# Performance work log

Hardware: AMD Instinct MI355X
Metric: run time of the kernel (lower is better)

The kernel has to match this reference:

```python
import jax, jax.numpy as jnp
import numpy as np

NUM_LEVELS = 16
BASE_RES = 16
MAX_RES = 2048
F_PER_LEVEL = 2
MAX_TABLE = 524288  # 2**19
N_POINTS = 1048576
# geometric resolution schedule, identical to the torch module
RESOLUTIONS = [int(BASE_RES * (MAX_RES / BASE_RES) ** (l / (NUM_LEVELS - 1))) for l in range(NUM_LEVELS)]
TABLE_SIZES = [min(r ** 3, MAX_TABLE) for r in RESOLUTIONS]


def setup_inputs() -> dict:
    key = jax.random.key(0)
    k0, k1, k2, k3 = jax.random.split(key, 4)
    coords = jax.random.uniform(k0, (N_POINTS, 3), minval=-1.0, maxval=1.0, dtype=jnp.float32)
    # hash tables init U(-1e-4, 1e-4); all padded to MAX_TABLE rows (levels with
    # smaller dense tables simply never index past TABLE_SIZES[l])
    tables = jax.random.uniform(k1, (NUM_LEVELS, MAX_TABLE, F_PER_LEVEL), minval=-1e-4, maxval=1e-4, dtype=jnp.float32)
    d_in = NUM_LEVELS * F_PER_LEVEL  # 32
    W1 = jax.random.normal(k2, (d_in, 128), dtype=jnp.float32) * (2.0 / (d_in + 128)) ** 0.5
    b1 = jnp.zeros((128,), dtype=jnp.float32)
    W2 = jax.random.normal(k3, (128, 64), dtype=jnp.float32) * (2.0 / (128 + 64)) ** 0.5
    b2 = jnp.zeros((64,), dtype=jnp.float32)
    return {"coords": coords, "tables": tables, "W1": W1, "b1": b1, "W2": W2, "b2": b2}


def _hash_gather(coords, tables):
    # coords: [N, 3] in [-1, 1] -> normalized to [0, 1]
    c = (coords + 1.0) * 0.5
    feats = []
    for l in range(NUM_LEVELS):
        R = RESOLUTIONS[l]
        T = TABLE_SIZES[l]
        d = jnp.clip(jnp.floor(c * R).astype(jnp.int32), 0, R - 1).astype(jnp.uint32)  # [N, 3]
        # (x*R^2 + y*R + z) % T in uint32. Wraparound mod 2^32 only occurs at the
        # finest levels where T = 2^19 divides 2^32, so the result stays exact.
        idx = (d[:, 0] * jnp.uint32(R * R) + d[:, 1] * jnp.uint32(R) + d[:, 2]) % jnp.uint32(T)
        feats.append(tables[l][idx.astype(jnp.int32)])  # [N, F_PER_LEVEL]
    return jnp.concatenate(feats, axis=-1)  # [N, 32], level-major


def reference(coords, tables, W1, b1, W2, b2):
    x = _hash_gather(coords, tables)              # [N, 32]
    h = jax.nn.relu(x @ W1 + b1)                  # [N, 128]
    return h @ W2 + b2                            # [N, 64]
```

## Files before the change

### kernel.cpp

```cpp
#include <hip/hip_runtime.h>
#include <stdint.h>


typedef __attribute__((ext_vector_type(8))) __bf16 bf16x8;
typedef __attribute__((ext_vector_type(4))) float  f32x4;
typedef __attribute__((ext_vector_type(2))) float  f32x2;

#define NPTS   1048576
#define NTILES 65536

__device__ __forceinline__ unsigned pack_bf16(float x, float y) {
  __bf16 a = (__bf16)x, b = (__bf16)y;
  unsigned short ua, ub;
  __builtin_memcpy(&ua, &a, 2);
  __builtin_memcpy(&ub, &b, 2);
  return (unsigned)ua | ((unsigned)ub << 16);
}

__global__ __launch_bounds__(256) void tconv_prep_kernel(
    const float* __restrict__ coords, const float* __restrict__ tables,
    const float* __restrict__ W1, const float* __restrict__ W2,
    unsigned* __restrict__ tb2, unsigned* __restrict__ xw,
    short* __restrict__ w1p, short* __restrict__ w2p)
{
  constexpr unsigned Rt[5] = {16u,22u,30u,42u,58u};
  if (blockIdx.x < 1024) {
    int p0 = blockIdx.x * 1024 + threadIdx.x;
#pragma unroll
    for (int i = 0; i < 4; ++i) {
      int p = p0 + (i << 8);
      float u0 = (coords[3*p+0] + 1.0f) * 0.5f;
      float u1 = (coords[3*p+1] + 1.0f) * 0.5f;
      float u2 = (coords[3*p+2] + 1.0f) * 0.5f;
#pragma unroll
      for (int lv = 0; lv < 5; ++lv) {
        const unsigned R = Rt[lv];
        const unsigned Rm1 = R - 1u;
        unsigned d0 = (unsigned)(int)(u0 * (float)R); if (d0 > Rm1) d0 = Rm1;
        unsigned d1 = (unsigned)(int)(u1 * (float)R); if (d1 > Rm1) d1 = Rm1;
        unsigned d2 = (unsigned)(int)(u2 * (float)R); if (d2 > Rm1) d2 = Rm1;
        unsigned idx = d0*(R*R) + d1*R + d2;
        f32x2 f = *(const f32x2*)(tables + ((size_t)lv << 20) + (size_t)idx*2u);
        xw[((size_t)lv << 20) + p] = pack_bf16(f.x, f.y);
      }
    }
    return;
  }
  if (blockIdx.x < 6656) {
    int e0 = 5*524288 + ((int)(blockIdx.x - 1024) * 256 + (int)threadIdx.x) * 4;
#pragma unroll
    for (int i = 0; i < 4; ++i) {
      int e = e0 + i;
      f32x2 f = *(const f32x2*)(tables + (size_t)e * 2);
      tb2[e] = pack_bf16(f.x, f.y);
    }
    return;
  }
  int tid = (blockIdx.x - 6656) * 256 + threadIdx.x;
  int l = tid & 63;
  int g = l >> 4;
  int c = l & 15;
  if (tid < 512) {
    int t = tid >> 6;
    bf16x8 v;
#pragma unroll
    for (int j = 0; j < 8; ++j)
      v[j] = (__bf16)W1[(8*g + j)*128 + 16*t + c];
    *(bf16x8*)(w1p + (size_t)(t*64 + l)*8) = v;
  } else if (tid < 1536) {
    int e = (tid - 512) >> 6;
    int mt = e >> 2, ks = e & 3;
    bf16x8 v;
#pragma unroll
    for (int j = 0; j < 8; ++j)
      v[j] = (__bf16)W2[(32*ks + 16*(j>>2) + 4*g + (j&3))*64 + 16*mt + c];
    *(bf16x8*)(w2p + (size_t)(e*64 + l)*8) = v;
  }
}

__global__ __launch_bounds__(256) void gather_kernel(
    const float* __restrict__ coords, const unsigned* __restrict__ tb2,
    unsigned* __restrict__ xw)
{
  constexpr unsigned Rt[16] = {16u,22u,30u,42u,58u,80u,111u,153u,
                               212u,294u,406u,561u,776u,1072u,1482u,2048u};
  const int xcd = blockIdx.x & 7;
  const int j   = blockIdx.x >> 3;
  int ghi = xcd * 1408 + j;
  int lv = 5 + (ghi >> 10);
  int chunk = ghi & 1023;

  const unsigned R = Rt[lv];
  const float fR = (float)R;
  const unsigned RR = R * R;
  const unsigned Rm1 = R - 1u;
  const unsigned M = (lv >= 6) ? 0x7FFFFu : 0xFFFFFFFFu;
  const unsigned* tb = tb2 + ((size_t)lv << 19);
  unsigned* xp = xw + ((size_t)lv << 20);

  int p0 = chunk * 1024 + threadIdx.x;
#pragma unroll
  for (int i = 0; i < 4; ++i) {
    int p = p0 + (i << 8);
    float u0 = (coords[3*p+0] + 1.0f) * 0.5f;
    float u1 = (coords[3*p+1] + 1.0f) * 0.5f;
    float u2 = (coords[3*p+2] + 1.0f) * 0.5f;
    unsigned d0 = (unsigned)(int)(u0 * fR); if (d0 > Rm1) d0 = Rm1;
    unsigned d1 = (unsigned)(int)(u1 * fR); if (d1 > Rm1) d1 = Rm1;
    unsigned d2 = (unsigned)(int)(u2 * fR); if (d2 > Rm1) d2 = Rm1;
    unsigned idx = (d0*RR + d1*R + d2) & M;
    xp[p] = tb[idx];
  }
}

__global__ __launch_bounds__(256, 4) void mlp_kernel(
    const unsigned* __restrict__ xw,
    const float* __restrict__ b1, const float* __restrict__ b2,
    const short* __restrict__ w1p, const short* __restrict__ w2p,
    float* __restrict__ out)
{
  const int l = threadIdx.x & 63;
  const int g = l >> 4;
  const int c = l & 15;
  const int w = threadIdx.x >> 6;

  __shared__ float obuf[4][16][68];

  bf16x8 w1f[8];
#pragma unroll
  for (int t = 0; t < 8; ++t)
    w1f[t] = *(const bf16x8*)(w1p + (size_t)(t*64 + l)*8);

  const int base = blockIdx.x * 4 + w;

  unsigned gx[2][4];
#pragma unroll
  for (int it = 0; it < 2; ++it) {
    int p = (base + it*32768)*16 + c;
#pragma unroll
    for (int q = 0; q < 4; ++q)
      gx[it][q] = xw[((size_t)(4*g + q) << 20) + p];
  }

#pragma unroll
  for (int it = 0; it < 2; ++it) {
    union { bf16x8 v; unsigned u[4]; } X;
#pragma unroll
    for (int q = 0; q < 4; ++q) X.u[q] = gx[it][q];
    bf16x8 xf = X.v;

    f32x4 h[8];
#pragma unroll
    for (int t = 0; t < 8; ++t) {
      h[t] = *(const f32x4*)(b1 + 16*t + 4*g);
      h[t] = __builtin_amdgcn_mfma_f32_16x16x32_bf16(w1f[t], xf, h[t], 0, 0, 0);
    }

    f32x4 o[4];
#pragma unroll
    for (int mt = 0; mt < 4; ++mt)
      o[mt] = *(const f32x4*)(b2 + 16*mt + 4*g);
#pragma unroll
    for (int ks = 0; ks < 4; ++ks) {
      bf16x8 bp;
#pragma unroll
      for (int j = 0; j < 8; ++j) {
        float v = h[2*ks + (j>>2)][j & 3];
        v = fmaxf(v, 0.0f);
        bp[j] = (__bf16)v;
      }
#pragma unroll
      for (int mt = 0; mt < 4; ++mt) {
        bf16x8 w2f = *(const bf16x8*)(w2p + (size_t)((mt*4 + ks)*64 + l)*8);
        o[mt] = __builtin_amdgcn_mfma_f32_16x16x32_bf16(w2f, bp, o[mt], 0, 0, 0);
      }
    }

    float (*ob)[68] = obuf[w];
#pragma unroll
    for (int mt = 0; mt < 4; ++mt)
      *(f32x4*)&ob[c][16*mt + 4*g] = o[mt];
    asm volatile("s_waitcnt lgkmcnt(0)" ::: "memory");
    f32x4 v[4];
#pragma unroll
    for (int s = 0; s < 4; ++s)
      v[s] = *(const f32x4*)&ob[4*s + g][4*c];
    asm volatile("" ::: "memory");
    float* op = out + (size_t)(base + it*32768) * 1024;
#pragma unroll
    for (int s = 0; s < 4; ++s)
      *(f32x4*)(op + (4*s + g)*64 + 4*c) = v[s];

    if (it < 1) asm volatile("s_waitcnt lgkmcnt(0)" ::: "memory");
  }
}

__global__ void prep_kernel(const float* __restrict__ W1, const float* __restrict__ W2,
                            short* __restrict__ w1p, short* __restrict__ w2p) {
  int tid = blockIdx.x * blockDim.x + threadIdx.x;
  int l = tid & 63;
  int g = l >> 4;
  int c = l & 15;
  if (tid < 512) {
    int t = tid >> 6;
    bf16x8 v;
#pragma unroll
    for (int j = 0; j < 8; ++j)
      v[j] = (__bf16)W1[(8*g + j)*128 + 16*t + c];
    *(bf16x8*)(w1p + (size_t)(t*64 + l)*8) = v;
  } else if (tid < 1536) {
    int e = (tid - 512) >> 6;
    int mt = e >> 2, ks = e & 3;
    bf16x8 v;
#pragma unroll
    for (int j = 0; j < 8; ++j)
      v[j] = (__bf16)W2[(32*ks + 16*(j>>2) + 4*g + (j&3))*64 + 16*mt + c];
    *(bf16x8*)(w2p + (size_t)(e*64 + l)*8) = v;
  }
}

__device__ const unsigned kRES[16] = {16u,22u,30u,42u,58u,80u,111u,153u,
                                      212u,294u,406u,561u,776u,1072u,1482u,2048u};

__global__ __launch_bounds__(256, 3) void hashgrid_mlp_kernel(
    const float* __restrict__ coords, const float* __restrict__ tables,
    const float* __restrict__ b1, const float* __restrict__ b2,
    const short* __restrict__ w1p, const short* __restrict__ w2p,
    float* __restrict__ out, int stride)
{
  const int l = threadIdx.x & 63;
  const int g = l >> 4;
  const int c = l & 15;

  unsigned Rq[4], RRq[4], Mq[4]; float fRq[4];
#pragma unroll
  for (int q = 0; q < 4; ++q) {
    int lv = 4*g + q;
    unsigned R = kRES[lv];
    Rq[q] = R; RRq[q] = R*R; fRq[q] = (float)R;
    Mq[q] = (lv >= 6) ? 0x7FFFFu : 0xFFFFFFFFu;
  }
  const float* tb = tables + ((size_t)g << 22);

  bf16x8 w1f[8];
#pragma unroll
  for (int t = 0; t < 8; ++t)
    w1f[t] = *(const bf16x8*)(w1p + (size_t)(t*64 + l)*8);

  f32x2 gx[4];
  auto prefetch = [&](int tile) {
    int p = tile*16 + c;
    float u0 = (coords[3*p+0] + 1.0f) * 0.5f;
    float u1 = (coords[3*p+1] + 1.0f) * 0.5f;
    float u2 = (coords[3*p+2] + 1.0f) * 0.5f;
#pragma unroll
    for (int q = 0; q < 4; ++q) {
      unsigned Rm1 = Rq[q] - 1u;
      unsigned d0 = (unsigned)(int)(u0 * fRq[q]); if (d0 > Rm1) d0 = Rm1;
      unsigned d1 = (unsigned)(int)(u1 * fRq[q]); if (d1 > Rm1) d1 = Rm1;
      unsigned d2 = (unsigned)(int)(u2 * fRq[q]); if (d2 > Rm1) d2 = Rm1;
      unsigned idx = (d0*RRq[q] + d1*Rq[q] + d2) & Mq[q];
      gx[q] = *(const f32x2*)(tb + ((size_t)q << 20) + (size_t)idx*2u);
    }
  };

  int tile = blockIdx.x * 4 + (threadIdx.x >> 6);
  prefetch(tile);
  while (true) {
    bf16x8 xf;
#pragma unroll
    for (int q = 0; q < 4; ++q) {
      xf[2*q]   = (__bf16)gx[q].x;
      xf[2*q+1] = (__bf16)gx[q].y;
    }
    int cur = tile;
    tile += stride;
    if (tile < NTILES) prefetch(tile);

    f32x4 h[8];
#pragma unroll
    for (int t = 0; t < 8; ++t) {
      h[t] = *(const f32x4*)(b1 + 16*t + 4*g);
      h[t] = __builtin_amdgcn_mfma_f32_16x16x32_bf16(w1f[t], xf, h[t], 0, 0, 0);
    }

    f32x4 o[4];
#pragma unroll
    for (int mt = 0; mt < 4; ++mt)
      o[mt] = *(const f32x4*)(b2 + 16*mt + 4*g);
#pragma unroll
    for (int ks = 0; ks < 4; ++ks) {
      bf16x8 bp;
#pragma unroll
      for (int j = 0; j < 8; ++j) {
        float v = h[2*ks + (j>>2)][j & 3];
        v = fmaxf(v, 0.0f);
        bp[j] = (__bf16)v;
      }
#pragma unroll
      for (int mt = 0; mt < 4; ++mt) {
        bf16x8 w2f = *(const bf16x8*)(w2p + (size_t)((mt*4 + ks)*64 + l)*8);
        o[mt] = __builtin_amdgcn_mfma_f32_16x16x32_bf16(w2f, bp, o[mt], 0, 0, 0);
      }
    }

    float* op = out + (size_t)(cur*16 + c)*64 + 4*g;
#pragma unroll
    for (int mt = 0; mt < 4; ++mt)
      *(f32x4*)(op + 16*mt) = o[mt];

    if (tile >= NTILES) break;
  }
}

extern "C" void kernel_launch(void* const* d_in, const int* in_sizes, int n_in,
                              void* d_out, int out_size, void* d_ws, size_t ws_size,
                              hipStream_t stream) {
  const float* coords = (const float*)d_in[0];
  const float* tables = (const float*)d_in[1];
  const float* W1     = (const float*)d_in[2];
  const float* b1     = (const float*)d_in[3];
  const float* W2     = (const float*)d_in[4];
  const float* b2     = (const float*)d_in[5];
  float* out = (float*)d_out;

  short* w1p = (short*)d_ws;
  short* w2p = w1p + 4096;

  const size_t XW_OFF  = 32*1024;
  const size_t XW_SZ   = (size_t)NPTS * 16 * 4;
  const size_t TB2_SZ  = (size_t)16 * 524288 * 4;
  const size_t need = XW_OFF + XW_SZ + TB2_SZ;

  if (ws_size >= need) {
    unsigned* xw  = (unsigned*)((char*)d_ws + XW_OFF);
    unsigned* tb2 = (unsigned*)((char*)d_ws + XW_OFF + XW_SZ);
    tconv_prep_kernel<<<6662, 256, 0, stream>>>(coords, tables, W1, W2,
                                                tb2, xw, w1p, w2p);
    gather_kernel<<<11264, 256, 0, stream>>>(coords, tb2, xw);
    mlp_kernel<<<8192, 256, 0, stream>>>(xw, b1, b2, w1p, w2p, out);
  } else {
    prep_kernel<<<6, 256, 0, stream>>>(W1, W2, w1p, w2p);
    const int blocks = 2048;
    hashgrid_mlp_kernel<<<blocks, 256, 0, stream>>>(coords, tables, b1, b2,
                                                    w1p, w2p, out, blocks*4);
  }
}
```

Baseline: 187.1 us.

## Fuse prep, gather and MLP into one cooperative kernel with slice pipelining

Replaces the three-kernel sequence with a single cooperative persistent kernel. It runs the table conversion and prep, then splits the points into four slices, so some blocks gather level features for slice s while the others run the MLP on slice s-1, with grid-wide syncs between phases. The aim is to overlap gather-bound memory traffic with MFMA work and to remove launch gaps between kernels. The cost is several grid syncs, a fixed split between gather and MLP blocks, and host-side attribute and occupancy queries on every launch. The fused single-pass fallback for small workspaces is removed, so that case now computes nothing.

```diff
diff --git a/kernel.cpp b/kernel.cpp
--- a/kernel.cpp
+++ b/kernel.cpp
@@ -1,13 +1,22 @@
 #include <hip/hip_runtime.h>
+#include <hip/hip_cooperative_groups.h>
 #include <stdint.h>
+
+namespace cg = cooperative_groups;
 
 
 typedef __attribute__((ext_vector_type(8))) __bf16 bf16x8;
 typedef __attribute__((ext_vector_type(4))) float  f32x4;
 typedef __attribute__((ext_vector_type(2))) float  f32x2;
 
-#define NPTS   1048576
-#define NTILES 65536
+#define NPTS        1048576
+#define NTILES      65536
+#define SLICE_PTS   262144
+#define SLICE_TILES 16384
+#define XCD_CHUNKS  352
+
+__device__ const unsigned kRES[16] = {16u,22u,30u,42u,58u,80u,111u,153u,
+                                      212u,294u,406u,561u,776u,1072u,1482u,2048u};
 
 __device__ __forceinline__ unsigned pack_bf16(float x, float y) {
   __bf16 a = (__bf16)x, b = (__bf16)y;
@@ -17,13 +26,204 @@
   return (unsigned)ua | ((unsigned)ub << 16);
 }
 
+__global__ __launch_bounds__(256) void mega_kernel(
+    const float* __restrict__ coords, const float* __restrict__ tables,
+    const float* __restrict__ W1, const float* __restrict__ b1,
+    const float* __restrict__ W2, const float* __restrict__ b2,
+    unsigned* __restrict__ tb2, unsigned* __restrict__ xw,
+    short* __restrict__ w1p, short* __restrict__ w2p,
+    float* __restrict__ out, int nper, int ng)
+{
+  cg::grid_group grid = cg::this_grid();
+  const int tid = threadIdx.x;
+  const int l = tid & 63;
+  const int g = l >> 4;
+  const int c = l & 15;
+  const int w = tid >> 6;
+  const int b = blockIdx.x;
+  const int x = b & 7;
+  const int r = b >> 3;
+  const int B = gridDim.x;
+
+  __shared__ float obuf[4][16][68];
+
+  for (int u = b; u < 6662; u += B) {
+    if (u < 1024) {
+      int p0 = u * 1024 + tid;
+#pragma unroll
+      for (int i = 0; i < 4; ++i) {
+        int p = p0 + (i << 8);
+        float u0 = (coords[3*p+0] + 1.0f) * 0.5f;
+        float u1 = (coords[3*p+1] + 1.0f) * 0.5f;
+        float u2 = (coords[3*p+2] + 1.0f) * 0.5f;
+#pragma unroll
+        for (int lv = 0; lv < 5; ++lv) {
+          const unsigned R = kRES[lv];
+          const unsigned Rm1 = R - 1u;
+          unsigned d0 = (unsigned)(int)(u0 * (float)R); if (d0 > Rm1) d0 = Rm1;
+          unsigned d1 = (unsigned)(int)(u1 * (float)R); if (d1 > Rm1) d1 = Rm1;
+          unsigned d2 = (unsigned)(int)(u2 * (float)R); if (d2 > Rm1) d2 = Rm1;
+          unsigned idx = d0*(R*R) + d1*R + d2;
+          f32x2 f = *(const f32x2*)(tables + ((size_t)lv << 20) + (size_t)idx*2u);
+          xw[((size_t)lv << 20) + p] = pack_bf16(f.x, f.y);
+        }
+      }
+    } else if (u < 6656) {
+      int e0 = 5*524288 + (u - 1024) * 1024 + tid * 4;
+#pragma unroll
+      for (int i = 0; i < 4; ++i) {
+        int e = e0 + i;
+        f32x2 f = *(const f32x2*)(tables + (size_t)e * 2);
+        tb2[e] = pack_bf16(f.x, f.y);
+      }
+    } else {
+      int t2 = (u - 6656) * 256 + tid;
+      if (t2 < 512) {
+        int t = t2 >> 6;
+        bf16x8 v;
+#pragma unroll
+        for (int j = 0; j < 8; ++j)
+          v[j] = (__bf16)W1[(8*g + j)*128 + 16*t + c];
+        *(bf16x8*)(w1p + (size_t)(t*64 + l)*8) = v;
+      } else if (t2 < 1536) {
+        int e = (t2 - 512) >> 6;
+        int mt = e >> 2, ks = e & 3;
+        bf16x8 v;
+#pragma unroll
+        for (int j = 0; j < 8; ++j)
+          v[j] = (__bf16)W2[(32*ks + 16*(j>>2) + 4*g + (j&3))*64 + 16*mt + c];
+        *(bf16x8*)(w2p + (size_t)(e*64 + l)*8) = v;
+      }
+    }
+  }
+
+  auto gather_slice = [&](int s, int rank, int stride) {
+    for (int h = rank; h < XCD_CHUNKS; h += stride) {
+      int hh = x * XCD_CHUNKS + h;
+      int lv = 5 + (hh >> 8);
+      int ch = hh & 255;
+      const unsigned R = kRES[lv];
+      const float fR = (float)R;
+      const unsigned RR = R * R;
+      const unsigned Rm1 = R - 1u;
+      const unsigned M = (lv >= 6) ? 0x7FFFFu : 0xFFFFFFFFu;
+      const unsigned* tb = tb2 + ((size_t)lv << 19);
+      unsigned* xp = xw + ((size_t)lv << 20);
+      int p0 = s * SLICE_PTS + ch * 1024 + tid;
+#pragma unroll
+      for (int i = 0; i < 4; ++i) {
+        int p = p0 + (i << 8);
+        float u0 = (coords[3*p+0] + 1.0f) * 0.5f;
+        float u1 = (coords[3*p+1] + 1.0f) * 0.5f;
+        float u2 = (coords[3*p+2] + 1.0f) * 0.5f;
+        unsigned d0 = (unsigned)(int)(u0 * fR); if (d0 > Rm1) d0 = Rm1;
+        unsigned d1 = (unsigned)(int)(u1 * fR); if (d1 > Rm1) d1 = Rm1;
+        unsigned d2 = (unsigned)(int)(u2 * fR); if (d2 > Rm1) d2 = Rm1;
+        unsigned idx = (d0*RR + d1*R + d2) & M;
+        xp[p] = tb[idx];
+      }
+    }
+  };
+
+  auto mlp_slice = [&](int s, int wid, int nwaves) {
+    bf16x8 w1f[8];
+#pragma unroll
+    for (int t = 0; t < 8; ++t)
+      w1f[t] = *(const bf16x8*)(w1p + (size_t)(t*64 + l)*8);
+
+    const int end = (s + 1) * SLICE_TILES;
+    int t = s * SLICE_TILES + wid;
+    if (t >= end) return;
+    unsigned gx[4];
+#pragma unroll
+    for (int q = 0; q < 4; ++q)
+      gx[q] = xw[((size_t)(4*g + q) << 20) + t*16 + c];
+
+    while (t < end) {
+      int nt = t + nwaves;
+      unsigned gx2[4];
+      if (nt < end) {
+#pragma unroll
+        for (int q = 0; q < 4; ++q)
+          gx2[q] = xw[((size_t)(4*g + q) << 20) + nt*16 + c];
+      }
+      union { bf16x8 v; unsigned u[4]; } X;
+#pragma unroll
+      for (int q = 0; q < 4; ++q) X.u[q] = gx[q];
+      bf16x8 xf = X.v;
+
+      f32x4 h[8];
+#pragma unroll
+      for (int tt = 0; tt < 8; ++tt) {
+        h[tt] = *(const f32x4*)(b1 + 16*tt + 4*g);
+        h[tt] = __builtin_amdgcn_mfma_f32_16x16x32_bf16(w1f[tt], xf, h[tt], 0, 0, 0);
+      }
+      f32x4 o[4];
+#pragma unroll
+      for (int mt = 0; mt < 4; ++mt)
+        o[mt] = *(const f32x4*)(b2 + 16*mt + 4*g);
+#pragma unroll
+      for (int ks = 0; ks < 4; ++ks) {
+        bf16x8 bp;
+#pragma unroll
+        for (int j = 0; j < 8; ++j) {
+          float v = h[2*ks + (j>>2)][j & 3];
+          v = fmaxf(v, 0.0f);
+          bp[j] = (__bf16)v;
+        }
+#pragma unroll
+        for (int mt = 0; mt < 4; ++mt) {
+          bf16x8 w2f = *(const bf16x8*)(w2p + (size_t)((mt*4 + ks)*64 + l)*8);
+          o[mt] = __builtin_amdgcn_mfma_f32_16x16x32_bf16(w2f, bp, o[mt], 0, 0, 0);
+        }
+      }
+      float (*ob)[68] = obuf[w];
+#pragma unroll
+      for (int mt = 0; mt < 4; ++mt)
+        *(f32x4*)&ob[c][16*mt + 4*g] = o[mt];
+      asm volatile("s_waitcnt lgkmcnt(0)" ::: "memory");
+      f32x4 v[4];
+#pragma unroll
+      for (int sdx = 0; sdx < 4; ++sdx)
+        v[sdx] = *(const f32x4*)&ob[4*sdx + g][4*c];
+      asm volatile("" ::: "memory");
+      float* op = out + (size_t)t * 1024;
+#pragma unroll
+      for (int sdx = 0; sdx < 4; ++sdx)
+        *(f32x4*)(op + (4*sdx + g)*64 + 4*c) = v[sdx];
+      asm volatile("s_waitcnt lgkmcnt(0)" ::: "memory");
+#pragma unroll
+      for (int q = 0; q < 4; ++q) gx[q] = gx2[q];
+      t = nt;
+    }
+  };
+
+  __threadfence();
+  grid.sync();
+
+  gather_slice(0, r, nper);
+  __threadfence();
+  grid.sync();
+
+  const int nm = nper - ng;
+  for (int s = 2; s <= 4; ++s) {
+    if (r < ng) gather_slice(s - 1, r, ng);
+    else        mlp_slice(s - 2, ((r - ng)*8 + x)*4 + w, 4*8*nm);
+    __threadfence();
+    grid.sync();
+  }
+  mlp_slice(3, (r*8 + x)*4 + w, 4*B);
+}
+
 __global__ __launch_bounds__(256) void tconv_prep_kernel(
     const float* __restrict__ coords, const float* __restrict__ tables,
     const float* __restrict__ W1, const float* __restrict__ W2,
     unsigned* __restrict__ tb2, unsigned* __restrict__ xw,
     short* __restrict__ w1p, short* __restrict__ w2p)
 {
-  constexpr unsigned Rt[5] = {16u,22u,30u,42u,58u};
+  const int l = threadIdx.x & 63;
+  const int g = l >> 4;
+  const int c = l & 15;
   if (blockIdx.x < 1024) {
     int p0 = blockIdx.x * 1024 + threadIdx.x;
 #pragma unroll
@@ -34,7 +234,7 @@
       float u2 = (coords[3*p+2] + 1.0f) * 0.5f;
 #pragma unroll
       for (int lv = 0; lv < 5; ++lv) {
-        const unsigned R = Rt[lv];
+        const unsigned R = kRES[lv];
         const unsigned Rm1 = R - 1u;
         unsigned d0 = (unsigned)(int)(u0 * (float)R); if (d0 > Rm1) d0 = Rm1;
         unsigned d1 = (unsigned)(int)(u1 * (float)R); if (d1 > Rm1) d1 = Rm1;
@@ -57,9 +257,6 @@
     return;
   }
   int tid = (blockIdx.x - 6656) * 256 + threadIdx.x;
-  int l = tid & 63;
-  int g = l >> 4;
-  int c = l & 15;
   if (tid < 512) {
     int t = tid >> 6;
     bf16x8 v;
@@ -82,22 +279,18 @@
     const float* __restrict__ coords, const unsigned* __restrict__ tb2,
     unsigned* __restrict__ xw)
 {
-  constexpr unsigned Rt[16] = {16u,22u,30u,42u,58u,80u,111u,153u,
-                               212u,294u,406u,561u,776u,1072u,1482u,2048u};
   const int xcd = blockIdx.x & 7;
   const int j   = blockIdx.x >> 3;
   int ghi = xcd * 1408 + j;
   int lv = 5 + (ghi >> 10);
   int chunk = ghi & 1023;
-
-  const unsigned R = Rt[lv];
+  const unsigned R = kRES[lv];
   const float fR = (float)R;
   const unsigned RR = R * R;
   const unsigned Rm1 = R - 1u;
   const unsigned M = (lv >= 6) ? 0x7FFFFu : 0xFFFFFFFFu;
   const unsigned* tb = tb2 + ((size_t)lv << 19);
   unsigned* xp = xw + ((size_t)lv << 20);
-
   int p0 = chunk * 1024 + threadIdx.x;
 #pragma unroll
   for (int i = 0; i < 4; ++i) {
@@ -123,16 +316,12 @@
   const int g = l >> 4;
   const int c = l & 15;
   const int w = threadIdx.x >> 6;
-
   __shared__ float obuf[4][16][68];
-
   bf16x8 w1f[8];
 #pragma unroll
   for (int t = 0; t < 8; ++t)
     w1f[t] = *(const bf16x8*)(w1p + (size_t)(t*64 + l)*8);
-
   const int base = blockIdx.x * 4 + w;
-
   unsigned gx[2][4];
 #pragma unroll
   for (int it = 0; it < 2; ++it) {
@@ -141,21 +330,18 @@
     for (int q = 0; q < 4; ++q)
       gx[it][q] = xw[((size_t)(4*g + q) << 20) + p];
   }
-
 #pragma unroll
   for (int it = 0; it < 2; ++it) {
     union { bf16x8 v; unsigned u[4]; } X;
 #pragma unroll
     for (int q = 0; q < 4; ++q) X.u[q] = gx[it][q];
     bf16x8 xf = X.v;
-
     f32x4 h[8];
 #pragma unroll
     for (int t = 0; t < 8; ++t) {
       h[t] = *(const f32x4*)(b1 + 16*t + 4*g);
       h[t] = __builtin_amdgcn_mfma_f32_16x16x32_bf16(w1f[t], xf, h[t], 0, 0, 0);
     }
-
     f32x4 o[4];
 #pragma unroll
     for (int mt = 0; mt < 4; ++mt)
@@ -175,7 +361,6 @@
         o[mt] = __builtin_amdgcn_mfma_f32_16x16x32_bf16(w2f, bp, o[mt], 0, 0, 0);
       }
     }
-
     float (*ob)[68] = obuf[w];
 #pragma unroll
     for (int mt = 0; mt < 4; ++mt)
@@ -190,126 +375,7 @@
 #pragma unroll
     for (int s = 0; s < 4; ++s)
       *(f32x4*)(op + (4*s + g)*64 + 4*c) = v[s];
-
     if (it < 1) asm volatile("s_waitcnt lgkmcnt(0)" ::: "memory");
-  }
-}
-
-__global__ void prep_kernel(const float* __restrict__ W1, const float* __restrict__ W2,
-                            short* __restrict__ w1p, short* __restrict__ w2p) {
-  int tid = blockIdx.x * blockDim.x + threadIdx.x;
-  int l = tid & 63;
-  int g = l >> 4;
-  int c = l & 15;
-  if (tid < 512) {
-    int t = tid >> 6;
-    bf16x8 v;
-#pragma unroll
-    for (int j = 0; j < 8; ++j)
-      v[j] = (__bf16)W1[(8*g + j)*128 + 16*t + c];
-    *(bf16x8*)(w1p + (size_t)(t*64 + l)*8) = v;
-  } else if (tid < 1536) {
-    int e = (tid - 512) >> 6;
-    int mt = e >> 2, ks = e & 3;
-    bf16x8 v;
-#pragma unroll
-    for (int j = 0; j < 8; ++j)
-      v[j] = (__bf16)W2[(32*ks + 16*(j>>2) + 4*g + (j&3))*64 + 16*mt + c];
-    *(bf16x8*)(w2p + (size_t)(e*64 + l)*8) = v;
-  }
-}
-
-__device__ const unsigned kRES[16] = {16u,22u,30u,42u,58u,80u,111u,153u,
-                                      212u,294u,406u,561u,776u,1072u,1482u,2048u};
-
-__global__ __launch_bounds__(256, 3) void hashgrid_mlp_kernel(
-    const float* __restrict__ coords, const float* __restrict__ tables,
-    const float* __restrict__ b1, const float* __restrict__ b2,
-    const short* __restrict__ w1p, const short* __restrict__ w2p,
-    float* __restrict__ out, int stride)
-{
-  const int l = threadIdx.x & 63;
-  const int g = l >> 4;
-  const int c = l & 15;
-
-  unsigned Rq[4], RRq[4], Mq[4]; float fRq[4];
-#pragma unroll
-  for (int q = 0; q < 4; ++q) {
-    int lv = 4*g + q;
-    unsigned R = kRES[lv];
-    Rq[q] = R; RRq[q] = R*R; fRq[q] = (float)R;
-    Mq[q] = (lv >= 6) ? 0x7FFFFu : 0xFFFFFFFFu;
-  }
-  const float* tb = tables + ((size_t)g << 22);
-
-  bf16x8 w1f[8];
-#pragma unroll
-  for (int t = 0; t < 8; ++t)
-    w1f[t] = *(const bf16x8*)(w1p + (size_t)(t*64 + l)*8);
-
-  f32x2 gx[4];
-  auto prefetch = [&](int tile) {
-    int p = tile*16 + c;
-    float u0 = (coords[3*p+0] + 1.0f) * 0.5f;
-    float u1 = (coords[3*p+1] + 1.0f) * 0.5f;
-    float u2 = (coords[3*p+2] + 1.0f) * 0.5f;
-#pragma unroll
-    for (int q = 0; q < 4; ++q) {
-      unsigned Rm1 = Rq[q] - 1u;
-      unsigned d0 = (unsigned)(int)(u0 * fRq[q]); if (d0 > Rm1) d0 = Rm1;
-      unsigned d1 = (unsigned)(int)(u1 * fRq[q]); if (d1 > Rm1) d1 = Rm1;
-      unsigned d2 = (unsigned)(int)(u2 * fRq[q]); if (d2 > Rm1) d2 = Rm1;
-      unsigned idx = (d0*RRq[q] + d1*Rq[q] + d2) & Mq[q];
-      gx[q] = *(const f32x2*)(tb + ((size_t)q << 20) + (size_t)idx*2u);
-    }
-  };
-
-  int tile = blockIdx.x * 4 + (threadIdx.x >> 6);
-  prefetch(tile);
-  while (true) {
-    bf16x8 xf;
-#pragma unroll
-    for (int q = 0; q < 4; ++q) {
-      xf[2*q]   = (__bf16)gx[q].x;
-      xf[2*q+1] = (__bf16)gx[q].y;
-    }
-    int cur = tile;
-    tile += stride;
-    if (tile < NTILES) prefetch(tile);
-
-    f32x4 h[8];
-#pragma unroll
-    for (int t = 0; t < 8; ++t) {
-      h[t] = *(const f32x4*)(b1 + 16*t + 4*g);
-      h[t] = __builtin_amdgcn_mfma_f32_16x16x32_bf16(w1f[t], xf, h[t], 0, 0, 0);
-    }
-
-    f32x4 o[4];
-#pragma unroll
-    for (int mt = 0; mt < 4; ++mt)
-      o[mt] = *(const f32x4*)(b2 + 16*mt + 4*g);
-#pragma unroll
-    for (int ks = 0; ks < 4; ++ks) {
-      bf16x8 bp;
-#pragma unroll
-      for (int j = 0; j < 8; ++j) {
-        float v = h[2*ks + (j>>2)][j & 3];
-        v = fmaxf(v, 0.0f);
-        bp[j] = (__bf16)v;
-      }
-#pragma unroll
-      for (int mt = 0; mt < 4; ++mt) {
-        bf16x8 w2f = *(const bf16x8*)(w2p + (size_t)((mt*4 + ks)*64 + l)*8);
-        o[mt] = __builtin_amdgcn_mfma_f32_16x16x32_bf16(w2f, bp, o[mt], 0, 0, 0);
-      }
-    }
-
-    float* op = out + (size_t)(cur*16 + c)*64 + 4*g;
-#pragma unroll
-    for (int mt = 0; mt < 4; ++mt)
-      *(f32x4*)(op + 16*mt) = o[mt];
-
-    if (tile >= NTILES) break;
   }
 }
 
@@ -330,19 +396,33 @@
   const size_t XW_OFF  = 32*1024;
   const size_t XW_SZ   = (size_t)NPTS * 16 * 4;
   const size_t TB2_SZ  = (size_t)16 * 524288 * 4;
-  const size_t need = XW_OFF + XW_SZ + TB2_SZ;
-
-  if (ws_size >= need) {
-    unsigned* xw  = (unsigned*)((char*)d_ws + XW_OFF);
-    unsigned* tb2 = (unsigned*)((char*)d_ws + XW_OFF + XW_SZ);
+  unsigned* xw  = (unsigned*)((char*)d_ws + XW_OFF);
+  unsigned* tb2 = (unsigned*)((char*)d_ws + XW_OFF + XW_SZ);
+
+  int dev = 0; hipGetDevice(&dev);
+  int coop = 0;
+  hipDeviceGetAttribute(&coop, hipDeviceAttributeCooperativeLaunch, dev);
+  int maxb = 0;
+  hipOccupancyMaxActiveBlocksPerMultiprocessor(&maxb, (const void*)mega_kernel, 256, 0);
+
+  if (ws_size >= XW_OFF + XW_SZ + TB2_SZ && coop && maxb > 0) {
+    if (maxb > 8) maxb = 8;
+    int B = maxb * 256;
+    if (B > 2048) B = 2048;
+    int nper = B / 8;
+    int ng = (9 * nper) / 16;
+    if (ng < 1) ng = 1;
+    if (ng > nper - 1) ng = nper - 1;
+    void* args[] = {(void*)&coords, (void*)&tables, (void*)&W1, (void*)&b1,
+                    (void*)&W2, (void*)&b2, (void*)&tb2, (void*)&xw,
+                    (void*)&w1p, (void*)&w2p, (void*)&out,
+                    (void*)&nper, (void*)&ng};
+    hipLaunchCooperativeKernel((void*)mega_kernel, dim3(B), dim3(256),
+                               args, 0, stream);
+  } else if (ws_size >= XW_OFF + XW_SZ + TB2_SZ) {
     tconv_prep_kernel<<<6662, 256, 0, stream>>>(coords, tables, W1, W2,
                                                 tb2, xw, w1p, w2p);
     gather_kernel<<<11264, 256, 0, stream>>>(coords, tb2, xw);
     mlp_kernel<<<8192, 256, 0, stream>>>(xw, b1, b2, w1p, w2p, out);
-  } else {
-    prep_kernel<<<6, 256, 0, stream>>>(W1, W2, w1p, w2p);
-    const int blocks = 2048;
-    hashgrid_mlp_kernel<<<blocks, 256, 0, stream>>>(coords, tables, b1, b2,
-                                                    w1p, w2p, out, blocks*4);
-  }
-}
+  }
+}
```

Result: no change. 187.5 us (+0.2%).
